# Kernel tuning notes

Hardware: AMD Instinct MI355X
Metric: run time of the kernel (lower is better)

## Reference

```python
import jax, jax.numpy as jnp
import numpy as np
import math

D_MODEL = 1024
NUM_HEADS = 16
THETA = 10000.0


def _rope(x, pos):
    # x: [B, H, S, d_k]; pos: [S] int -- complex rotation on interleaved pairs
    d_k = x.shape[-1]
    inv_freq = 1.0 / (THETA ** (jnp.arange(0, d_k, 2, dtype=jnp.float32) / d_k))  # [d_k/2]
    angles = pos.astype(jnp.float32)[:, None] * inv_freq[None, :]  # [S, d_k/2]
    cos, sin = jnp.cos(angles), jnp.sin(angles)
    xe = x[..., 0::2]  # real parts
    xo = x[..., 1::2]  # imag parts
    out = jnp.stack([xe * cos - xo * sin, xe * sin + xo * cos], axis=-1)
    return out.reshape(x.shape)


def setup_inputs() -> dict:
    key = jax.random.key(0)
    k1, k2, k3 = jax.random.split(key, 3)
    B, S, D = 2, 2048, D_MODEL
    w_std = math.sqrt(2.0 / (D + 3 * D))
    o_std = math.sqrt(2.0 / (D + D))
    return {
        "x": jax.random.normal(k1, (B, S, D), dtype=jnp.float32),
        "token_positions": jnp.arange(S, dtype=jnp.int32),
        "w_qkv": jax.random.normal(k2, (3 * D, D), dtype=jnp.float32) * w_std,
        "w_out": jax.random.normal(k3, (D, D), dtype=jnp.float32) * o_std,
    }


def reference(x, token_positions, w_qkv, w_out):
    B, S, D = x.shape
    H = NUM_HEADS
    d_k = D // H

    qkv = jnp.einsum('bsd,ed->bse', x, w_qkv)  # [B, S, 3D]
    q, k, v = jnp.split(qkv, 3, axis=-1)

    def to_heads(t):
        return t.reshape(B, S, H, d_k).transpose(0, 2, 1, 3)  # [B, H, S, d_k]

    q, k, v = to_heads(q), to_heads(k), to_heads(v)
    q = _rope(q, token_positions)
    k = _rope(k, token_positions)

    scores = jnp.einsum('bhqd,bhkd->bhqk', q, k) / math.sqrt(d_k)
    causal = jnp.tril(jnp.ones((S, S), dtype=bool))
    scores = jnp.where(causal, scores, -jnp.inf)
    attn = jax.nn.softmax(scores, axis=-1)
    out = jnp.einsum('bhqk,bhkd->bhqd', attn, v)  # [B, H, S, d_k]
    out = out.transpose(0, 2, 1, 3).reshape(B, S, D)
    return jnp.einsum('bsd,ed->bse', out, w_out)
```

## Files before the change

kernel.cpp:

```cpp
#include <hip/hip_runtime.h>

typedef unsigned short u16;
typedef unsigned int u32;
typedef __attribute__((ext_vector_type(8))) __bf16 bf16x8;
typedef __attribute__((ext_vector_type(4))) float f32x4;
typedef __attribute__((ext_vector_type(4))) u32 u32x4;
typedef __attribute__((ext_vector_type(4))) u16 u16x4;

#define DEV __device__ __forceinline__

constexpr int S_LEN = 2048;
constexpr int DMODEL = 1024;
constexpr int NHEAD = 16;
constexpr int EX = 3072;
constexpr int ROWS = 4096;
constexpr float QSCALE = 0.125f * 1.4426950408889634f;

DEV u16 f2bf(float f) {
  union { float f; u32 u; } v; v.f = f;
  u32 u = v.u;
  u32 r = (u + 0x7fffu + ((u >> 16) & 1u)) >> 16;
  return (u16)r;
}
DEV float bf2f(u32 lo16) {
  union { u32 u; float f; } v; v.u = lo16 << 16; return v.f;
}
DEV float vexp2(float x) {
#if __has_builtin(__builtin_amdgcn_exp2f)
  return __builtin_amdgcn_exp2f(x);
#else
  return exp2f(x);
#endif
}
DEV void gload_lds16(const u16* g, u16* l) {
  __builtin_amdgcn_global_load_lds((const __attribute__((address_space(1))) void*)g,
                                   (__attribute__((address_space(3))) void*)l, 16, 0, 0);
}
DEV int swz(int r, int c) { return r * 64 + (c ^ ((r & 7) << 3)); }

__global__ __launch_bounds__(256) void k_cvt_all(const float* __restrict__ x,
                                                 const float* __restrict__ wq,
                                                 const float* __restrict__ wo,
                                                 u16* __restrict__ xb,
                                                 u16* __restrict__ wqb,
                                                 u16* __restrict__ wob) {
  int i = blockIdx.x * 256 + threadIdx.x;
  const float* in; u16* out; int off;
  if (i < 524288)       { in = x;  out = xb;  off = i; }
  else if (i < 917504)  { in = wq; out = wqb; off = i - 524288; }
  else                  { in = wo; out = wob; off = i - 917504; }
  const float4* p4 = (const float4*)in;
  float4 a = p4[2 * off], b = p4[2 * off + 1];
  alignas(16) u16 r[8] = {f2bf(a.x), f2bf(a.y), f2bf(a.z), f2bf(a.w),
                          f2bf(b.x), f2bf(b.y), f2bf(b.z), f2bf(b.w)};
  *(u32x4*)(out + 8 * off) = *(const u32x4*)r;
}

__global__ __launch_bounds__(256) void k_rope_tab(const int* __restrict__ pos,
                                                  float* __restrict__ ctab,
                                                  float* __restrict__ stab) {
  int t = blockIdx.x * 256 + threadIdx.x;
  int s = t >> 5, fi = t & 31;
  float p = (float)pos[s];
  float invf = expf(-(float)fi * 0.28782313662425572f);
  float ang = p * invf;
  ctab[t] = cosf(ang);
  stab[t] = sinf(ang);
}

__global__ __launch_bounds__(256) void k_rope(u16* __restrict__ qk,
                                              const float* __restrict__ ctab,
                                              const float* __restrict__ stab) {
  int idx = blockIdx.x * 256 + threadIdx.x;
  int row = idx >> 10, rem = idx & 1023;
  int p = rem >> 9, hfi = rem & 511;
  int h = hfi >> 5, fi = hfi & 31;
  int s = row & (S_LEN - 1);
  u32* ptr = (u32*)(qk + (size_t)row * 2048 + p * 1024 + h * 64 + 2 * fi);
  u32 v = *ptr;
  float xe = bf2f(v & 0xffffu), xo = bf2f(v >> 16);
  float c = ctab[s * 32 + fi], sn = stab[s * 32 + fi];
  float scl = (p == 0) ? QSCALE : 1.0f;
  u32 lo = (u32)f2bf((xe * c - xo * sn) * scl);
  u32 hi = (u32)f2bf((xe * sn + xo * c) * scl);
  *ptr = lo | (hi << 16);
}

template <int MODE>
__global__ __launch_bounds__(256) void k_gemm_bt(const u16* __restrict__ A,
                                                 const u16* __restrict__ Bw,
                                                 void* __restrict__ Out,
                                                 u16* __restrict__ vt,
                                                 int M, int N, int K) {
  __shared__ alignas(16) u16 As[128 * 32];
  __shared__ alignas(16) u16 Bs[128 * 32];
  const int tid = threadIdx.x, lane = tid & 63;
  const int w = tid >> 6, wr = w >> 1, wc = w & 1;
  const int l15 = lane & 15, l16 = lane >> 4;
  const int m0 = blockIdx.x * 128, n0 = blockIdx.y * 128;
  f32x4 acc[4][4] = {};
  const int grow = w * 32 + (lane >> 2);
  const int gcol = (lane & 3) * 8;
  const int ldst = w * 1024 + lane * 8;

  for (int k0 = 0; k0 < K; k0 += 32) {
    __syncthreads();
#pragma unroll
    for (int i = 0; i < 2; i++) {
      gload_lds16(&A[(size_t)(m0 + grow + i * 16) * K + k0 + gcol], &As[ldst + i * 512]);
      gload_lds16(&Bw[(size_t)(n0 + grow + i * 16) * K + k0 + gcol], &Bs[ldst + i * 512]);
    }
    __syncthreads();
    bf16x8 af[4], bfr[4];
#pragma unroll
    for (int m = 0; m < 4; m++) af[m] = *(const bf16x8*)&As[(wr * 64 + m * 16 + l15) * 32 + l16 * 8];
#pragma unroll
    for (int n = 0; n < 4; n++) bfr[n] = *(const bf16x8*)&Bs[(wc * 64 + n * 16 + l15) * 32 + l16 * 8];
#pragma unroll
    for (int m = 0; m < 4; m++)
#pragma unroll
      for (int n = 0; n < 4; n++)
        acc[m][n] = __builtin_amdgcn_mfma_f32_16x16x32_bf16(af[m], bfr[n], acc[m][n], 0, 0, 0);
  }

  const int rb = m0 + wr * 64 + l16 * 4;
  const int cb = n0 + wc * 64 + l15;
  if (MODE == 1 && n0 >= 2048) {
#pragma unroll
    for (int m = 0; m < 4; m++)
#pragma unroll
      for (int n = 0; n < 4; n++) {
        int row = rb + m * 16;
        int col = cb + n * 16;
        int bb = row >> 11, s = row & 2047, hd = col - 2048;
        u16x4 pk = {f2bf(acc[m][n][0]), f2bf(acc[m][n][1]),
                    f2bf(acc[m][n][2]), f2bf(acc[m][n][3])};
        *(u16x4*)&vt[(size_t)(bb * 1024 + hd) * S_LEN + s] = pk;
      }
  } else {
#pragma unroll
    for (int m = 0; m < 4; m++)
#pragma unroll
      for (int n = 0; n < 4; n++)
#pragma unroll
        for (int r = 0; r < 4; r++) {
          int row = rb + m * 16 + r, col = cb + n * 16;
          if (MODE == 1)
            ((u16*)Out)[(size_t)row * 2048 + col] = f2bf(acc[m][n][r]);
          else
            ((float*)Out)[(size_t)row * N + col] = acc[m][n][r];
        }
  }
}

__global__ __launch_bounds__(256) void k_attn(const u16* __restrict__ qk,
                                              const u16* __restrict__ vt,
                                              u16* __restrict__ aout) {
  __shared__ alignas(16) u16 Ks[64 * 64];
  __shared__ alignas(16) u16 Vs[64 * 64];
  __shared__ alignas(16) u16 Ps[4][16 * 64];
  const int tid = threadIdx.x, lane = tid & 63, w = tid >> 6;
  const int l15 = lane & 15, l16 = lane >> 4;
  const int qt = 31 - blockIdx.y;
  const int q0 = qt * 64;
  const int bh = blockIdx.x, b = bh >> 4, h = bh & 15;
  const u16* qbase = qk + (size_t)b * S_LEN * 2048 + h * 64;
  const u16* kbase = qbase + 1024;
  const u16* vbase = vt + (size_t)bh * 64 * S_LEN;
  const int wq0 = q0 + w * 16;

  bf16x8 qa[2];
#pragma unroll
  for (int kb = 0; kb < 2; kb++)
    qa[kb] = *(const bf16x8*)&qbase[(size_t)(wq0 + l15) * 2048 + kb * 32 + l16 * 8];

  bf16x8 vone;
#pragma unroll
  for (int j = 0; j < 8; j++) vone[j] = (__bf16)1.0f;

  f32x4 osum[4] = {};
  f32x4 osl = {};

  const int nt = qt + 1;
  const int srow = tid >> 2, scg = (tid & 3) * 16;
  u32x4 kr0, kr1, vr0, vr1;
  {
    const u16* kp = kbase + (size_t)srow * 2048 + scg;
    kr0 = *(const u32x4*)kp; kr1 = *(const u32x4*)(kp + 8);
    const u16* vp = vbase + (size_t)srow * S_LEN + scg;
    vr0 = *(const u32x4*)vp; vr1 = *(const u32x4*)(vp + 8);
  }

  for (int t = 0; t < nt; t++) {
    const int kv0 = t * 64;
    __syncthreads();
    *(u32x4*)&Ks[swz(srow, scg)]     = kr0;
    *(u32x4*)&Ks[swz(srow, scg + 8)] = kr1;
    *(u32x4*)&Vs[swz(srow, scg)]     = vr0;
    *(u32x4*)&Vs[swz(srow, scg + 8)] = vr1;
    __syncthreads();
    if (t + 1 < nt) {
      const u16* kp = kbase + (size_t)(kv0 + 64 + srow) * 2048 + scg;
      kr0 = *(const u32x4*)kp; kr1 = *(const u32x4*)(kp + 8);
      const u16* vp = vbase + (size_t)srow * S_LEN + kv0 + 64 + scg;
      vr0 = *(const u32x4*)vp; vr1 = *(const u32x4*)(vp + 8);
    }

    f32x4 sc[4];
#pragma unroll
    for (int n = 0; n < 4; n++) {
      bf16x8 kf0 = *(const bf16x8*)&Ks[swz(n * 16 + l15, l16 * 8)];
      bf16x8 kf1 = *(const bf16x8*)&Ks[swz(n * 16 + l15, 32 + l16 * 8)];
      f32x4 z = {0.f, 0.f, 0.f, 0.f};
      z = __builtin_amdgcn_mfma_f32_16x16x32_bf16(qa[0], kf0, z, 0, 0, 0);
      sc[n] = __builtin_amdgcn_mfma_f32_16x16x32_bf16(qa[1], kf1, z, 0, 0, 0);
    }

    const bool diag = (t == nt - 1);
#pragma unroll
    for (int n = 0; n < 4; n++)
#pragma unroll
      for (int r = 0; r < 4; r++) {
        float s = sc[n][r];
        if (diag && (kv0 + n * 16 + l15 > wq0 + l16 * 4 + r)) s = -1e30f;
        float p = vexp2(s - 16.0f);
        Ps[w][swz(l16 * 4 + r, n * 16 + l15)] = f2bf(p);
      }

#pragma unroll
    for (int ks = 0; ks < 2; ks++) {
      bf16x8 pa = *(const bf16x8*)&Ps[w][swz(l15, ks * 32 + l16 * 8)];
      osl = __builtin_amdgcn_mfma_f32_16x16x32_bf16(pa, vone, osl, 0, 0, 0);
#pragma unroll
      for (int n = 0; n < 4; n++) {
        bf16x8 vb = *(const bf16x8*)&Vs[swz(n * 16 + l15, ks * 32 + l16 * 8)];
        osum[n] = __builtin_amdgcn_mfma_f32_16x16x32_bf16(pa, vb, osum[n], 0, 0, 0);
      }
    }
  }

  f32x4 inv;
#pragma unroll
  for (int r = 0; r < 4; r++) inv[r] = 1.0f / osl[r];
  u16* ob = aout + (size_t)b * S_LEN * DMODEL + h * 64;
#pragma unroll
  for (int n = 0; n < 4; n++)
#pragma unroll
    for (int r = 0; r < 4; r++) {
      int s = wq0 + l16 * 4 + r;
      ob[(size_t)s * DMODEL + n * 16 + l15] = f2bf(osum[n][r] * inv[r]);
    }
}

extern "C" void kernel_launch(void* const* d_in, const int* in_sizes, int n_in,
                              void* d_out, int out_size, void* d_ws, size_t ws_size,
                              hipStream_t stream) {
  const float* x = (const float*)d_in[0];
  const int* pos = (const int*)d_in[1];
  const float* wqkv = (const float*)d_in[2];
  const float* wout = (const float*)d_in[3];
  float* out = (float*)d_out;
  char* ws = (char*)d_ws;

  u16* qkb  = (u16*)(ws);
  u16* vtb  = (u16*)(ws + 16777216);
  u16* aoutb = (u16*)(ws + 25165824);
  u16* xb   = (u16*)(ws + 33554432);
  u16* wqb  = (u16*)(ws + 41943040);
  u16* wob  = (u16*)(ws + 48234496);
  float* ctab = (float*)(ws + 50331648);
  float* stab = (float*)(ws + 50593792);
  (void)ws_size;

  k_cvt_all<<<4096, 256, 0, stream>>>(x, wqkv, wout, xb, wqb, wob);
  k_rope_tab<<<65536 / 256, 256, 0, stream>>>(pos, ctab, stab);

  dim3 g1(ROWS / 128, EX / 128);
  k_gemm_bt<1><<<g1, 256, 0, stream>>>(xb, wqb, qkb, vtb, ROWS, EX, DMODEL);

  k_rope<<<(ROWS * 1024) / 256, 256, 0, stream>>>(qkb, ctab, stab);

  dim3 ga(2 * NHEAD, S_LEN / 64);
  k_attn<<<ga, 256, 0, stream>>>(qkb, vtb, aoutb);

  dim3 g2(ROWS / 128, DMODEL / 128);
  k_gemm_bt<0><<<g2, 256, 0, stream>>>(aoutb, wob, out, nullptr, ROWS, DMODEL, DMODEL);
}
```

Baseline: 119.7 us.

## Replace QKV projection GEMM with 256x256 tiled, 8-wave, phase-pipelined kernel

Adds a dedicated QKV GEMM kernel using 256x256 output tiles, 512 threads and double-buffered LDS with XOR-swizzled layout. Each K step is split into four phases that interleave async global-to-LDS staging with MFMA blocks under explicit waitcnt and barriers, with setprio raised around the MFMAs. The goal is more data reuse per tile and overlap of memory traffic with matrix math. The cost is fewer blocks (192) on a large GPU, which risks poor occupancy and tail effects, plus heavy reliance on hand-tuned synchronisation. The old generic GEMM loses its V-transpose epilogue since it now only serves the output projection.

```diff
diff --git a/kernel.cpp b/kernel.cpp
--- a/kernel.cpp
+++ b/kernel.cpp
@@ -86,6 +86,143 @@
   *ptr = lo | (hi << 16);
 }
 
+__global__ __launch_bounds__(512, 2) void k_gemm1_8ph(const u16* __restrict__ A,
+                                                      const u16* __restrict__ Bw,
+                                                      u16* __restrict__ qk,
+                                                      u16* __restrict__ vt) {
+  __shared__ alignas(16) u16 Asm[2][2][8192];
+  __shared__ alignas(16) u16 Bsm[2][2][8192];
+  const int tid = threadIdx.x;
+  const int lane = tid & 63, l15 = lane & 15, l16 = lane >> 4;
+  const int w = tid >> 6, wr = w >> 2, wc = w & 3;
+  const int m0 = blockIdx.x * 256, n0 = blockIdx.y * 256;
+
+  const int sr = tid >> 3, gg = tid & 7;
+  const int swcol = ((gg ^ (sr & 7)) * 8);
+  const u16* aS = A + (size_t)(m0 + sr) * 1024 + swcol;
+  const u16* bS = Bw + (size_t)(n0 + sr) * 1024 + swcol;
+  const int ldst = tid * 8;
+
+#define STAGE_A(T, h) do { \
+    const u16* s_ = aS + (size_t)((h) * 128) * 1024 + (T) * 64; \
+    u16* d_ = &Asm[(T) & 1][(h)][ldst]; \
+    gload_lds16(s_, d_); \
+    gload_lds16(s_ + 64 * 1024, d_ + 4096); \
+  } while (0)
+#define STAGE_B(T, h) do { \
+    const u16* s_ = bS + (size_t)((h) * 128) * 1024 + (T) * 64; \
+    u16* d_ = &Bsm[(T) & 1][(h)][ldst]; \
+    gload_lds16(s_, d_); \
+    gload_lds16(s_ + 64 * 1024, d_ + 4096); \
+  } while (0)
+
+  const int xr = l15 & 7;
+  const int offK0 = l15 * 64 + ((l16 ^ xr) * 8);
+  const int offK1 = l15 * 64 + (((4 + l16) ^ xr) * 8);
+  const int brow = (wc & 1) * 64;
+
+  f32x4 acc[8][4] = {};
+
+  STAGE_A(0, 0); STAGE_A(0, 1);
+  STAGE_B(0, 0); STAGE_B(0, 1);
+  STAGE_A(1, 0); STAGE_A(1, 1);
+
+#define PHASE_SYNC() do { \
+    asm volatile("s_waitcnt lgkmcnt(0)" ::: "memory"); \
+    asm volatile("s_barrier" ::: "memory"); \
+    __builtin_amdgcn_sched_barrier(0); \
+  } while (0)
+#define MFMA16(mh, nh) do { \
+    __builtin_amdgcn_s_setprio(1); \
+    _Pragma("unroll") \
+    for (int m_ = 0; m_ < 4; m_++) \
+      _Pragma("unroll") \
+      for (int j_ = 0; j_ < 2; j_++) \
+        _Pragma("unroll") \
+        for (int k_ = 0; k_ < 2; k_++) \
+          acc[(mh) * 4 + m_][(nh) * 2 + j_] = __builtin_amdgcn_mfma_f32_16x16x32_bf16( \
+              Ar[mh][m_][k_], Br[j_][k_], acc[(mh) * 4 + m_][(nh) * 2 + j_], 0, 0, 0); \
+    __builtin_amdgcn_s_setprio(0); \
+    asm volatile("s_barrier" ::: "memory"); \
+    __builtin_amdgcn_sched_barrier(0); \
+  } while (0)
+
+  for (int T = 0; T < 16; ++T) {
+    if (T < 15) asm volatile("s_waitcnt vmcnt(4)" ::: "memory");
+    else        asm volatile("s_waitcnt vmcnt(0)" ::: "memory");
+    asm volatile("s_barrier" ::: "memory");
+    __builtin_amdgcn_sched_barrier(0);
+    const u16* Ab = &Asm[T & 1][wr][0];
+    const u16* Bb = &Bsm[T & 1][wc >> 1][0];
+    bf16x8 Ar[2][4][2], Br[2][2];
+
+#pragma unroll
+    for (int m = 0; m < 4; m++) {
+      Ar[0][m][0] = *(const bf16x8*)&Ab[(m * 16) * 64 + offK0];
+      Ar[0][m][1] = *(const bf16x8*)&Ab[(m * 16) * 64 + offK1];
+    }
+#pragma unroll
+    for (int j = 0; j < 2; j++) {
+      Br[j][0] = *(const bf16x8*)&Bb[(brow + j * 16) * 64 + offK0];
+      Br[j][1] = *(const bf16x8*)&Bb[(brow + j * 16) * 64 + offK1];
+    }
+    if (T + 1 < 16) STAGE_B(T + 1, 0);
+    PHASE_SYNC();
+    MFMA16(0, 0);
+
+#pragma unroll
+    for (int m = 0; m < 4; m++) {
+      Ar[1][m][0] = *(const bf16x8*)&Ab[(64 + m * 16) * 64 + offK0];
+      Ar[1][m][1] = *(const bf16x8*)&Ab[(64 + m * 16) * 64 + offK1];
+    }
+    if (T + 1 < 16) STAGE_B(T + 1, 1);
+    PHASE_SYNC();
+    MFMA16(1, 0);
+
+#pragma unroll
+    for (int j = 0; j < 2; j++) {
+      Br[j][0] = *(const bf16x8*)&Bb[(brow + 32 + j * 16) * 64 + offK0];
+      Br[j][1] = *(const bf16x8*)&Bb[(brow + 32 + j * 16) * 64 + offK1];
+    }
+    if (T + 2 < 16) STAGE_A(T + 2, 0);
+    PHASE_SYNC();
+    MFMA16(0, 1);
+
+    if (T + 2 < 16) STAGE_A(T + 2, 1);
+    PHASE_SYNC();
+    MFMA16(1, 1);
+  }
+
+  const int rb = m0 + wr * 128 + l16 * 4;
+  const int cb = n0 + wc * 64 + l15;
+  if (n0 < 2048) {
+#pragma unroll
+    for (int m = 0; m < 8; m++)
+#pragma unroll
+      for (int n = 0; n < 4; n++)
+#pragma unroll
+        for (int r = 0; r < 4; r++) {
+          int row = rb + m * 16 + r, col = cb + n * 16;
+          qk[(size_t)row * 2048 + col] = f2bf(acc[m][n][r]);
+        }
+  } else {
+#pragma unroll
+    for (int m = 0; m < 8; m++)
+#pragma unroll
+      for (int n = 0; n < 4; n++) {
+        int row = rb + m * 16, col = cb + n * 16;
+        int bb = row >> 11, s = row & 2047, hd = col - 2048;
+        u16x4 pk = {f2bf(acc[m][n][0]), f2bf(acc[m][n][1]),
+                    f2bf(acc[m][n][2]), f2bf(acc[m][n][3])};
+        *(u16x4*)&vt[(size_t)(bb * 1024 + hd) * 2048 + s] = pk;
+      }
+  }
+#undef STAGE_A
+#undef STAGE_B
+#undef PHASE_SYNC
+#undef MFMA16
+}
+
 template <int MODE>
 __global__ __launch_bounds__(256) void k_gemm_bt(const u16* __restrict__ A,
                                                  const u16* __restrict__ Bw,
@@ -125,32 +262,18 @@
 
   const int rb = m0 + wr * 64 + l16 * 4;
   const int cb = n0 + wc * 64 + l15;
-  if (MODE == 1 && n0 >= 2048) {
-#pragma unroll
-    for (int m = 0; m < 4; m++)
-#pragma unroll
-      for (int n = 0; n < 4; n++) {
-        int row = rb + m * 16;
-        int col = cb + n * 16;
-        int bb = row >> 11, s = row & 2047, hd = col - 2048;
-        u16x4 pk = {f2bf(acc[m][n][0]), f2bf(acc[m][n][1]),
-                    f2bf(acc[m][n][2]), f2bf(acc[m][n][3])};
-        *(u16x4*)&vt[(size_t)(bb * 1024 + hd) * S_LEN + s] = pk;
+#pragma unroll
+  for (int m = 0; m < 4; m++)
+#pragma unroll
+    for (int n = 0; n < 4; n++)
+#pragma unroll
+      for (int r = 0; r < 4; r++) {
+        int row = rb + m * 16 + r, col = cb + n * 16;
+        if (MODE == 1)
+          ((u16*)Out)[(size_t)row * 2048 + col] = f2bf(acc[m][n][r]);
+        else
+          ((float*)Out)[(size_t)row * N + col] = acc[m][n][r];
       }
-  } else {
-#pragma unroll
-    for (int m = 0; m < 4; m++)
-#pragma unroll
-      for (int n = 0; n < 4; n++)
-#pragma unroll
-        for (int r = 0; r < 4; r++) {
-          int row = rb + m * 16 + r, col = cb + n * 16;
-          if (MODE == 1)
-            ((u16*)Out)[(size_t)row * 2048 + col] = f2bf(acc[m][n][r]);
-          else
-            ((float*)Out)[(size_t)row * N + col] = acc[m][n][r];
-        }
-  }
 }
 
 __global__ __launch_bounds__(256) void k_attn(const u16* __restrict__ qk,
@@ -275,8 +398,8 @@
   k_cvt_all<<<4096, 256, 0, stream>>>(x, wqkv, wout, xb, wqb, wob);
   k_rope_tab<<<65536 / 256, 256, 0, stream>>>(pos, ctab, stab);
 
-  dim3 g1(ROWS / 128, EX / 128);
-  k_gemm_bt<1><<<g1, 256, 0, stream>>>(xb, wqb, qkb, vtb, ROWS, EX, DMODEL);
+  dim3 g1(ROWS / 256, EX / 256);
+  k_gemm1_8ph<<<g1, 512, 0, stream>>>(xb, wqb, qkb, vtb);
 
   k_rope<<<(ROWS * 1024) / 256, 256, 0, stream>>>(qkb, ctab, stab);
 
```

New measurement: 125.4 us. 4.7% more time.

## Double-buffer GEMM with BK=64 swizzled LDS, XCD remap, and fuse RoPE into epilogue

Applied to the files above, without the earlier changes.

Rewrites the GEMM with a double-buffered K=64 swizzled LDS pipeline, so the next tile's global-to-LDS loads overlap MFMA work. It also raises MFMA priority and remaps block IDs across the 8 XCDs for better L2 locality. The separate RoPE kernel is removed: RoPE and the Q scaling are applied in the QKV GEMM epilogue using a lane shuffle to pair even and odd columns. The cos/sin table becomes an interleaved float2 array. LDS use grows to 64KB per block, which may limit occupancy.

```diff
diff --git a/kernel.cpp b/kernel.cpp
--- a/kernel.cpp
+++ b/kernel.cpp
@@ -12,7 +12,6 @@
 constexpr int S_LEN = 2048;
 constexpr int DMODEL = 1024;
 constexpr int NHEAD = 16;
-constexpr int EX = 3072;
 constexpr int ROWS = 4096;
 constexpr float QSCALE = 0.125f * 1.4426950408889634f;
 
@@ -21,9 +20,6 @@
   u32 u = v.u;
   u32 r = (u + 0x7fffu + ((u >> 16) & 1u)) >> 16;
   return (u16)r;
-}
-DEV float bf2f(u32 lo16) {
-  union { u32 u; float f; } v; v.u = lo16 << 16; return v.f;
 }
 DEV float vexp2(float x) {
 #if __has_builtin(__builtin_amdgcn_exp2f)
@@ -57,99 +53,147 @@
 }
 
 __global__ __launch_bounds__(256) void k_rope_tab(const int* __restrict__ pos,
-                                                  float* __restrict__ ctab,
-                                                  float* __restrict__ stab) {
+                                                  float2* __restrict__ tab) {
   int t = blockIdx.x * 256 + threadIdx.x;
   int s = t >> 5, fi = t & 31;
   float p = (float)pos[s];
   float invf = expf(-(float)fi * 0.28782313662425572f);
   float ang = p * invf;
-  ctab[t] = cosf(ang);
-  stab[t] = sinf(ang);
-}
-
-__global__ __launch_bounds__(256) void k_rope(u16* __restrict__ qk,
-                                              const float* __restrict__ ctab,
-                                              const float* __restrict__ stab) {
-  int idx = blockIdx.x * 256 + threadIdx.x;
-  int row = idx >> 10, rem = idx & 1023;
-  int p = rem >> 9, hfi = rem & 511;
-  int h = hfi >> 5, fi = hfi & 31;
-  int s = row & (S_LEN - 1);
-  u32* ptr = (u32*)(qk + (size_t)row * 2048 + p * 1024 + h * 64 + 2 * fi);
-  u32 v = *ptr;
-  float xe = bf2f(v & 0xffffu), xo = bf2f(v >> 16);
-  float c = ctab[s * 32 + fi], sn = stab[s * 32 + fi];
-  float scl = (p == 0) ? QSCALE : 1.0f;
-  u32 lo = (u32)f2bf((xe * c - xo * sn) * scl);
-  u32 hi = (u32)f2bf((xe * sn + xo * c) * scl);
-  *ptr = lo | (hi << 16);
+  tab[t] = float2{cosf(ang), sinf(ang)};
 }
 
 template <int MODE>
-__global__ __launch_bounds__(256) void k_gemm_bt(const u16* __restrict__ A,
+__global__ __launch_bounds__(256, 2) void k_gemm(const u16* __restrict__ A,
                                                  const u16* __restrict__ Bw,
                                                  void* __restrict__ Out,
                                                  u16* __restrict__ vt,
-                                                 int M, int N, int K) {
-  __shared__ alignas(16) u16 As[128 * 32];
-  __shared__ alignas(16) u16 Bs[128 * 32];
+                                                 const float2* __restrict__ tab,
+                                                 int NB) {
+  __shared__ alignas(16) u16 As[2][8192];
+  __shared__ alignas(16) u16 Bs[2][8192];
   const int tid = threadIdx.x, lane = tid & 63;
   const int w = tid >> 6, wr = w >> 1, wc = w & 1;
   const int l15 = lane & 15, l16 = lane >> 4;
-  const int m0 = blockIdx.x * 128, n0 = blockIdx.y * 128;
+  const int cpx = gridDim.x >> 3;
+  const int wg = (blockIdx.x & 7) * cpx + (blockIdx.x >> 3);
+  const int mb = wg / NB, nb = wg - mb * NB;
+  const int m0 = mb * 128, n0 = nb * 128;
+
+  const int sr = tid >> 3;
+  const int swcol = ((tid & 7) ^ (sr & 7)) * 8;
+  const u16* aT = A + (size_t)(m0 + sr) * 1024 + swcol;
+  const u16* bT = Bw + (size_t)(n0 + sr) * 1024 + swcol;
+  const int dst0 = tid * 8;
+
+#define STAGE(bufc, t) do { \
+    _Pragma("unroll") \
+    for (int i_ = 0; i_ < 4; i_++) { \
+      gload_lds16(aT + (size_t)(i_ * 32) * 1024 + (t) * 64, &As[bufc][dst0 + i_ * 2048]); \
+      gload_lds16(bT + (size_t)(i_ * 32) * 1024 + (t) * 64, &Bs[bufc][dst0 + i_ * 2048]); \
+    } \
+  } while (0)
+
   f32x4 acc[4][4] = {};
-  const int grow = w * 32 + (lane >> 2);
-  const int gcol = (lane & 3) * 8;
-  const int ldst = w * 1024 + lane * 8;
-
-  for (int k0 = 0; k0 < K; k0 += 32) {
-    __syncthreads();
-#pragma unroll
-    for (int i = 0; i < 2; i++) {
-      gload_lds16(&A[(size_t)(m0 + grow + i * 16) * K + k0 + gcol], &As[ldst + i * 512]);
-      gload_lds16(&Bw[(size_t)(n0 + grow + i * 16) * K + k0 + gcol], &Bs[ldst + i * 512]);
-    }
-    __syncthreads();
-    bf16x8 af[4], bfr[4];
-#pragma unroll
-    for (int m = 0; m < 4; m++) af[m] = *(const bf16x8*)&As[(wr * 64 + m * 16 + l15) * 32 + l16 * 8];
-#pragma unroll
-    for (int n = 0; n < 4; n++) bfr[n] = *(const bf16x8*)&Bs[(wc * 64 + n * 16 + l15) * 32 + l16 * 8];
-#pragma unroll
-    for (int m = 0; m < 4; m++)
-#pragma unroll
-      for (int n = 0; n < 4; n++)
-        acc[m][n] = __builtin_amdgcn_mfma_f32_16x16x32_bf16(af[m], bfr[n], acc[m][n], 0, 0, 0);
+  const int x7 = l15 & 7;
+
+#define COMPUTE(bufc) do { \
+    bf16x8 af_[4][2], bf_[4][2]; \
+    _Pragma("unroll") \
+    for (int m_ = 0; m_ < 4; m_++) \
+      _Pragma("unroll") \
+      for (int k_ = 0; k_ < 2; k_++) \
+        af_[m_][k_] = *(const bf16x8*)&As[bufc][(wr * 64 + m_ * 16 + l15) * 64 + \
+                                               (((k_ * 4 + l16) ^ x7) * 8)]; \
+    _Pragma("unroll") \
+    for (int n_ = 0; n_ < 4; n_++) \
+      _Pragma("unroll") \
+      for (int k_ = 0; k_ < 2; k_++) \
+        bf_[n_][k_] = *(const bf16x8*)&Bs[bufc][(wc * 64 + n_ * 16 + l15) * 64 + \
+                                               (((k_ * 4 + l16) ^ x7) * 8)]; \
+    __builtin_amdgcn_s_setprio(1); \
+    _Pragma("unroll") \
+    for (int m_ = 0; m_ < 4; m_++) \
+      _Pragma("unroll") \
+      for (int n_ = 0; n_ < 4; n_++) \
+        _Pragma("unroll") \
+        for (int k_ = 0; k_ < 2; k_++) \
+          acc[m_][n_] = __builtin_amdgcn_mfma_f32_16x16x32_bf16( \
+              af_[m_][k_], bf_[n_][k_], acc[m_][n_], 0, 0, 0); \
+    __builtin_amdgcn_s_setprio(0); \
+  } while (0)
+
+#define VMBAR() do { \
+    asm volatile("s_waitcnt vmcnt(0)" ::: "memory"); \
+    asm volatile("s_barrier" ::: "memory"); \
+  } while (0)
+
+  STAGE(0, 0);
+  VMBAR();
+  for (int t = 0; t < 16; t += 2) {
+    STAGE(1, t + 1);
+    COMPUTE(0);
+    VMBAR();
+    if (t + 2 < 16) {
+      STAGE(0, t + 2);
+      COMPUTE(1);
+      VMBAR();
+    } else {
+      COMPUTE(1);
+    }
   }
+#undef STAGE
+#undef COMPUTE
+#undef VMBAR
 
   const int rb = m0 + wr * 64 + l16 * 4;
   const int cb = n0 + wc * 64 + l15;
-  if (MODE == 1 && n0 >= 2048) {
+  if (MODE == 0) {
+    float* o = (float*)Out;
 #pragma unroll
     for (int m = 0; m < 4; m++)
 #pragma unroll
+      for (int n = 0; n < 4; n++)
+#pragma unroll
+        for (int r = 0; r < 4; r++)
+          o[(size_t)(rb + m * 16 + r) * 1024 + cb + n * 16] = acc[m][n][r];
+  } else if (n0 >= 2048) {
+#pragma unroll
+    for (int m = 0; m < 4; m++)
+#pragma unroll
       for (int n = 0; n < 4; n++) {
-        int row = rb + m * 16;
-        int col = cb + n * 16;
+        int row = rb + m * 16, col = cb + n * 16;
         int bb = row >> 11, s = row & 2047, hd = col - 2048;
         u16x4 pk = {f2bf(acc[m][n][0]), f2bf(acc[m][n][1]),
                     f2bf(acc[m][n][2]), f2bf(acc[m][n][3])};
         *(u16x4*)&vt[(size_t)(bb * 1024 + hd) * S_LEN + s] = pk;
       }
   } else {
-#pragma unroll
-    for (int m = 0; m < 4; m++)
-#pragma unroll
-      for (int n = 0; n < 4; n++)
+    u16* qk = (u16*)Out;
+    const bool isq = (n0 < 1024);
+#pragma unroll
+    for (int m = 0; m < 4; m++) {
+      int row0 = rb + m * 16;
+      int s0 = row0 & 2047;
+#pragma unroll
+      for (int n = 0; n < 4; n++) {
+        int col = cb + n * 16;
+        int fi = (col & 63) >> 1;
+        bool odd = col & 1;
+        f32x4 v = acc[m][n];
+        f32x4 p;
+#pragma unroll
+        for (int r = 0; r < 4; r++) p[r] = __shfl_xor(v[r], 1);
 #pragma unroll
         for (int r = 0; r < 4; r++) {
-          int row = rb + m * 16 + r, col = cb + n * 16;
-          if (MODE == 1)
-            ((u16*)Out)[(size_t)row * 2048 + col] = f2bf(acc[m][n][r]);
-          else
-            ((float*)Out)[(size_t)row * N + col] = acc[m][n][r];
+          float2 cs = tab[(s0 + r) * 32 + fi];
+          float xe = odd ? p[r] : v[r];
+          float xo = odd ? v[r] : p[r];
+          float o = odd ? (xe * cs.y + xo * cs.x) : (xe * cs.x - xo * cs.y);
+          if (isq) o *= QSCALE;
+          qk[(size_t)(row0 + r) * 2048 + col] = f2bf(o);
         }
+      }
+    }
   }
 }
 
@@ -262,27 +306,22 @@
   float* out = (float*)d_out;
   char* ws = (char*)d_ws;
 
-  u16* qkb  = (u16*)(ws);
-  u16* vtb  = (u16*)(ws + 16777216);
+  u16* qkb   = (u16*)(ws);
+  u16* vtb   = (u16*)(ws + 16777216);
   u16* aoutb = (u16*)(ws + 25165824);
-  u16* xb   = (u16*)(ws + 33554432);
-  u16* wqb  = (u16*)(ws + 41943040);
-  u16* wob  = (u16*)(ws + 48234496);
-  float* ctab = (float*)(ws + 50331648);
-  float* stab = (float*)(ws + 50593792);
+  u16* xb    = (u16*)(ws + 33554432);
+  u16* wqb   = (u16*)(ws + 41943040);
+  u16* wob   = (u16*)(ws + 48234496);
+  float2* tab = (float2*)(ws + 50331648);
   (void)ws_size;
 
   k_cvt_all<<<4096, 256, 0, stream>>>(x, wqkv, wout, xb, wqb, wob);
-  k_rope_tab<<<65536 / 256, 256, 0, stream>>>(pos, ctab, stab);
-
-  dim3 g1(ROWS / 128, EX / 128);
-  k_gemm_bt<1><<<g1, 256, 0, stream>>>(xb, wqb, qkb, vtb, ROWS, EX, DMODEL);
-
-  k_rope<<<(ROWS * 1024) / 256, 256, 0, stream>>>(qkb, ctab, stab);
+  k_rope_tab<<<65536 / 256, 256, 0, stream>>>(pos, tab);
+
+  k_gemm<1><<<768, 256, 0, stream>>>(xb, wqb, qkb, vtb, tab, 24);
 
   dim3 ga(2 * NHEAD, S_LEN / 64);
   k_attn<<<ga, 256, 0, stream>>>(qkb, vtb, aoutb);
 
-  dim3 g2(ROWS / 128, DMODEL / 128);
-  k_gemm_bt<0><<<g2, 256, 0, stream>>>(aoutb, wob, out, nullptr, ROWS, DMODEL, DMODEL);
-}
+  k_gemm<0><<<256, 256, 0, stream>>>(aoutb, wob, out, nullptr, nullptr, 8);
+}
```

New measurement: 103.8 us. -13.3%, faster.
